# Optimization experiments

Measured on AMD Instinct MI355X. Metric: run time of the kernel, lower is better.

## Reference

```python
import jax, jax.numpy as jnp
import numpy as np

NUM_HEADS = 16
GROUP_SIZE = 4


def setup_inputs() -> dict:
    key = jax.random.key(0)
    k1, k2, k3 = jax.random.split(key, 3)
    B, N, C = 4, 8192, 1024
    x = jax.random.normal(k1, (B, N, C), dtype=jnp.float32)
    w_qkv = jax.random.normal(k2, (C, 3 * C), dtype=jnp.float32) * (C ** -0.5)
    w_proj = jax.random.normal(k3, (C, C), dtype=jnp.float32) * (C ** -0.5)
    b_proj = jnp.zeros((C,), dtype=jnp.float32)
    return {"x": x, "w_qkv": w_qkv, "w_proj": w_proj, "b_proj": b_proj, "causal": 0}


def reference(x, w_qkv, w_proj, b_proj, causal):
    # NOTE: the original non-flash path ignores `causal` (no mask applied).
    B, N, C = x.shape
    H, Dh, g = NUM_HEADS, C // NUM_HEADS, GROUP_SIZE
    G = N // g
    scale = Dh ** -0.5
    qkv = (x @ w_qkv).reshape(B, N, 3, H, Dh)
    q, k, v = qkv[:, :, 0], qkv[:, :, 1], qkv[:, :, 2]  # [B, N, H, Dh]
    # split sequence into G contiguous groups of size g
    q = q.reshape(B, G, g, H, Dh) * scale
    k = k.reshape(B, G, g, H, Dh)
    v = v.reshape(B, G, g, H, Dh)
    attn = jnp.einsum('bgnhd,bgmhd->bghnm', q, k)  # [B, G, H, g, g]
    attn = jax.nn.softmax(attn, axis=-1)
    o = jnp.einsum('bghnm,bgmhd->bgnhd', attn, v)  # [B, G, g, H, Dh]
    o = o.reshape(B, N, C)
    return o @ w_proj + b_proj
```

## Files before the change

kernel.cpp:

```cpp
#include <hip/hip_runtime.h>
#include <hip/hip_bf16.h>
#include <hip/hip_fp16.h>


typedef float    f32x4 __attribute__((ext_vector_type(4)));
typedef _Float16 f16x8 __attribute__((ext_vector_type(8)));
typedef _Float16 f16x4 __attribute__((ext_vector_type(4)));

__device__ __forceinline__ void gload16(const _Float16* g, _Float16* l) {
  __builtin_amdgcn_global_load_lds((const __attribute__((address_space(1))) void*)g,
                                   (__attribute__((address_space(3))) void*)l,
                                   16, 0, 0);
}

__global__ void wsplit_kernel(const float* __restrict__ W,
                              _Float16* __restrict__ BTh,
                              _Float16* __restrict__ BTl, int N) {
  __shared__ float tile[64][65];
  int n0 = blockIdx.x * 64;
  int k0 = blockIdx.y * 64;
  int t  = threadIdx.x;
  int tr = t >> 4, tc = t & 15;
#pragma unroll
  for (int it = 0; it < 4; ++it) {
    int k = k0 + tr + it * 16;
    f32x4 v = *reinterpret_cast<const f32x4*>(W + (size_t)k * N + n0 + (tc << 2));
#pragma unroll
    for (int c = 0; c < 4; ++c) tile[tr + it * 16][(tc << 2) + c] = v[c];
  }
  __syncthreads();
#pragma unroll
  for (int it = 0; it < 4; ++it) {
    int n = n0 + tr + it * 16;
    f16x4 hi, lo;
#pragma unroll
    for (int c = 0; c < 4; ++c) {
      float f = tile[(tc << 2) + c][tr + it * 16];
      _Float16 h = (_Float16)f;
      hi[c] = h;
      lo[c] = (_Float16)(f - (float)h);
    }
    size_t off = (size_t)n * 1024 + k0 + (tc << 2);
    *reinterpret_cast<f16x4*>(BTh + off) = hi;
    *reinterpret_cast<f16x4*>(BTl + off) = lo;
  }
}

__launch_bounds__(256)
__global__ void gemm_split_kernel(const float* __restrict__ A,
                                  const _Float16* __restrict__ Bh,
                                  const _Float16* __restrict__ Bl,
                                  float* __restrict__ C,
                                  const float* __restrict__ bias,
                                  int M, int N, int lda, int ldc) {
  __shared__ _Float16 lAh[128 * 32];
  __shared__ _Float16 lAl[128 * 32];
  __shared__ _Float16 lBh[128 * 32];
  __shared__ _Float16 lBl[128 * 32];

  int nwg = gridDim.x, bid = blockIdx.x;
  int q8  = nwg >> 3;
  int swz = (bid & 7) * q8 + (bid >> 3);
  int Mt  = M >> 7;
  int tm  = swz % Mt, tn = swz / Mt;
  int brow = tm << 7, bcol = tn << 7;

  int t  = threadIdx.x;
  int wv = t >> 6, lane = t & 63;
  int wrow = (wv >> 1) << 6;
  int wcol = (wv & 1) << 6;
  int lr = lane & 15, kb = lane >> 4;

  const float* paf = A + (size_t)(brow + (t >> 3)) * lda + ((t & 7) << 2);
  _Float16* wAh = lAh + (t >> 3) * 32 + ((t & 7) << 2);
  _Float16* wAl = lAl + (t >> 3) * 32 + ((t & 7) << 2);

  const _Float16* pbh0 = Bh + (size_t)(bcol + (t >> 2)) * 1024 + ((t & 3) << 3);
  const _Float16* pbh1 = pbh0 + (size_t)64 * 1024;
  const _Float16* pbl0 = Bl + (size_t)(bcol + (t >> 2)) * 1024 + ((t & 3) << 3);
  const _Float16* pbl1 = pbl0 + (size_t)64 * 1024;
  _Float16* lBh0 = lBh + wv * 512;
  _Float16* lBh1 = lBh + 2048 + wv * 512;
  _Float16* lBl0 = lBl + wv * 512;
  _Float16* lBl1 = lBl + 2048 + wv * 512;

  const _Float16* arh = lAh + (wrow + lr) * 32 + kb * 8;
  const _Float16* arl = lAl + (wrow + lr) * 32 + kb * 8;
  const _Float16* brh = lBh + (wcol + lr) * 32 + kb * 8;
  const _Float16* brl = lBl + (wcol + lr) * 32 + kb * 8;

  f32x4 acc[4][4] = {};

  for (int kt = 0; kt < 1024; kt += 32) {
#pragma unroll
    for (int p = 0; p < 4; ++p) {
      f32x4 v = *reinterpret_cast<const f32x4*>(paf + (size_t)(p * 32) * lda + kt);
      f16x4 h, l;
#pragma unroll
      for (int c = 0; c < 4; ++c) {
        _Float16 hh = (_Float16)v[c];
        h[c] = hh;
        l[c] = (_Float16)(v[c] - (float)hh);
      }
      *reinterpret_cast<f16x4*>(wAh + p * 1024) = h;
      *reinterpret_cast<f16x4*>(wAl + p * 1024) = l;
    }
    gload16(pbh0 + kt, lBh0);
    gload16(pbh1 + kt, lBh1);
    gload16(pbl0 + kt, lBl0);
    gload16(pbl1 + kt, lBl1);
    __syncthreads();

    f16x8 ah[4], al[4], bh[4], bl[4];
#pragma unroll
    for (int i = 0; i < 4; ++i) {
      ah[i] = *reinterpret_cast<const f16x8*>(arh + i * 512);
      al[i] = *reinterpret_cast<const f16x8*>(arl + i * 512);
      bh[i] = *reinterpret_cast<const f16x8*>(brh + i * 512);
      bl[i] = *reinterpret_cast<const f16x8*>(brl + i * 512);
    }
#pragma unroll
    for (int mi = 0; mi < 4; ++mi)
#pragma unroll
      for (int ni = 0; ni < 4; ++ni) {
        acc[mi][ni] = __builtin_amdgcn_mfma_f32_16x16x32_f16(ah[mi], bh[ni], acc[mi][ni], 0, 0, 0);
        acc[mi][ni] = __builtin_amdgcn_mfma_f32_16x16x32_f16(al[mi], bh[ni], acc[mi][ni], 0, 0, 0);
        acc[mi][ni] = __builtin_amdgcn_mfma_f32_16x16x32_f16(ah[mi], bl[ni], acc[mi][ni], 0, 0, 0);
      }
    __syncthreads();
  }

  int crow0 = brow + wrow + (kb << 2);
  int ccol0 = bcol + wcol + lr;
#pragma unroll
  for (int ni = 0; ni < 4; ++ni) {
    int col = ccol0 + (ni << 4);
    float bv = bias ? bias[col] : 0.0f;
#pragma unroll
    for (int mi = 0; mi < 4; ++mi) {
#pragma unroll
      for (int r = 0; r < 4; ++r) {
        int row = crow0 + (mi << 4) + r;
        C[(size_t)row * ldc + col] = acc[mi][ni][r] + bv;
      }
    }
  }
}

__global__ void attn_kernel(float* __restrict__ qkv) {
  int u    = (blockIdx.x << 2) + (threadIdx.x >> 6);
  int lane = threadIdx.x & 63;
  int j  = lane >> 4;
  int tq = lane & 15;
  int h   = u & 15;
  int grp = u >> 4;
  size_t row = (size_t)grp * 4 + j;
  size_t idx = row * 3072 + h * 64 + (tq << 2);

  f32x4 qv = *reinterpret_cast<const f32x4*>(qkv + idx);
  f32x4 kv = *reinterpret_cast<const f32x4*>(qkv + idx + 1024);
  f32x4 vv = *reinterpret_cast<const f32x4*>(qkv + idx + 2048);
  qv *= 0.125f;

  float s[4];
#pragma unroll
  for (int e = 0; e < 4; ++e) {
    f32x4 ke;
    if (e == 0) ke = kv;
    else {
#pragma unroll
      for (int c = 0; c < 4; ++c) ke[c] = __shfl_xor(kv[c], e << 4);
    }
    float p = qv[0]*ke[0] + qv[1]*ke[1] + qv[2]*ke[2] + qv[3]*ke[3];
    p += __shfl_xor(p, 1);
    p += __shfl_xor(p, 2);
    p += __shfl_xor(p, 4);
    p += __shfl_xor(p, 8);
    s[e] = p;
  }
  float mx = fmaxf(fmaxf(s[0], s[1]), fmaxf(s[2], s[3]));
  float e0 = expf(s[0] - mx), e1 = expf(s[1] - mx), e2 = expf(s[2] - mx), e3 = expf(s[3] - mx);
  float inv = 1.0f / (e0 + e1 + e2 + e3);
  float P[4] = {e0 * inv, e1 * inv, e2 * inv, e3 * inv};

  f32x4 o = {0.0f, 0.0f, 0.0f, 0.0f};
#pragma unroll
  for (int e = 0; e < 4; ++e) {
    f32x4 ve;
    if (e == 0) ve = vv;
    else {
#pragma unroll
      for (int c = 0; c < 4; ++c) ve[c] = __shfl_xor(vv[c], e << 4);
    }
    o += P[e] * ve;
  }

  *reinterpret_cast<f32x4*>(qkv + idx) = o;
}

extern "C" void kernel_launch(void* const* d_in, const int* in_sizes, int n_in,
                              void* d_out, int out_size, void* d_ws, size_t ws_size,
                              hipStream_t stream) {
  const float* x      = (const float*)d_in[0];
  const float* w_qkv  = (const float*)d_in[1];
  const float* w_proj = (const float*)d_in[2];
  const float* b_proj = (const float*)d_in[3];
  float* out = (float*)d_out;
  char* ws = (char*)d_ws;

  int Ms;
  if      (ws_size >= 117440512ull) Ms = 8192;
  else if (ws_size >=  41943040ull) Ms = 2048;
  else                              Ms = 512;
  const int SL = 32768 / Ms;

  size_t qkvBytes = (size_t)Ms * 3072 * 4;
  float*    QKVs = (float*)ws;
  _Float16* Bqh  = (_Float16*)(ws + qkvBytes);
  _Float16* Bql  = (_Float16*)(ws + qkvBytes + 6291456ull);
  _Float16* Bph  = (_Float16*)(ws + qkvBytes + 12582912ull);
  _Float16* Bpl  = (_Float16*)(ws + qkvBytes + 14680064ull);

  wsplit_kernel<<<dim3(48, 16), 256, 0, stream>>>(w_qkv, Bqh, Bql, 3072);
  wsplit_kernel<<<dim3(16, 16), 256, 0, stream>>>(w_proj, Bph, Bpl, 1024);

  for (int s = 0; s < SL; ++s) {
    const float* xs = x + (size_t)s * Ms * 1024;
    gemm_split_kernel<<<(Ms >> 7) * 24, 256, 0, stream>>>(
        xs, Bqh, Bql, QKVs, nullptr, Ms, 3072, 1024, 3072);
    attn_kernel<<<Ms, 256, 0, stream>>>(QKVs);
    gemm_split_kernel<<<(Ms >> 7) * 8, 256, 0, stream>>>(
        QKVs, Bph, Bpl, out + (size_t)s * Ms * 1024, b_proj, Ms, 1024, 3072, 1024);
  }
}
```

Measured before the change: 1.195 ms.

## Presplit activations to fp16 hi/lo and add pipelined 256x256 QKV GEMM

Adds a pre-pass that splits x into interleaved fp16 hi/lo planes, so the QKV GEMM no longer converts fp32 inside its main loop. The QKV GEMM is replaced by a 512-thread, 256x256-tile kernel with 4-slot LDS multi-buffering, swizzled LDS layout, explicit vmcnt waits and setprio around MFMA. The 3-term split product runs as a 48-step K loop over the concatenated hi/lo planes. Attention now writes its output directly as fp16 hi/lo for the projection GEMM, and the projection GEMM does three sequential passes over the planes. The workspace chunk sizes are also changed, and the extra split pass costs additional memory traffic.

Measured after the change: 1.623 ms. +35.8%, slower.

```diff
diff --git a/kernel.cpp b/kernel.cpp
--- a/kernel.cpp
+++ b/kernel.cpp
@@ -13,14 +13,29 @@
                                    16, 0, 0);
 }
 
+#define FULL_BAR() do { asm volatile("" ::: "memory"); \
+  __builtin_amdgcn_s_barrier(); asm volatile("" ::: "memory"); } while (0)
+
+__global__ void presplit_kernel(const float* __restrict__ x, _Float16* __restrict__ XA) {
+  int gid = blockIdx.x * 256 + threadIdx.x;
+  int row = gid >> 8, c4 = gid & 255;
+  f32x4 v = *reinterpret_cast<const f32x4*>(x + ((size_t)gid << 2));
+  f16x4 hi, lo;
+#pragma unroll
+  for (int c = 0; c < 4; ++c) {
+    _Float16 h = (_Float16)v[c];
+    hi[c] = h; lo[c] = (_Float16)(v[c] - (float)h);
+  }
+  size_t o = (size_t)row * 2048 + (c4 << 2);
+  *reinterpret_cast<f16x4*>(XA + o)        = hi;
+  *reinterpret_cast<f16x4*>(XA + o + 1024) = lo;
+}
+
 __global__ void wsplit_kernel(const float* __restrict__ W,
-                              _Float16* __restrict__ BTh,
-                              _Float16* __restrict__ BTl, int N) {
+                              _Float16* __restrict__ BT, int N) {
   __shared__ float tile[64][65];
-  int n0 = blockIdx.x * 64;
-  int k0 = blockIdx.y * 64;
-  int t  = threadIdx.x;
-  int tr = t >> 4, tc = t & 15;
+  int n0 = blockIdx.x * 64, k0 = blockIdx.y * 64;
+  int t = threadIdx.x, tr = t >> 4, tc = t & 15;
 #pragma unroll
   for (int it = 0; it < 4; ++it) {
     int k = k0 + tr + it * 16;
@@ -37,97 +52,193 @@
     for (int c = 0; c < 4; ++c) {
       float f = tile[(tc << 2) + c][tr + it * 16];
       _Float16 h = (_Float16)f;
-      hi[c] = h;
-      lo[c] = (_Float16)(f - (float)h);
-    }
-    size_t off = (size_t)n * 1024 + k0 + (tc << 2);
-    *reinterpret_cast<f16x4*>(BTh + off) = hi;
-    *reinterpret_cast<f16x4*>(BTl + off) = lo;
-  }
+      hi[c] = h; lo[c] = (_Float16)(f - (float)h);
+    }
+    size_t off = (size_t)n * 2048 + k0 + (tc << 2);
+    *reinterpret_cast<f16x4*>(BT + off)        = hi;
+    *reinterpret_cast<f16x4*>(BT + off + 1024) = lo;
+  }
+}
+
+__launch_bounds__(512, 1)
+__global__ void gemm8_kernel(const _Float16* __restrict__ A,
+                             const _Float16* __restrict__ B,
+                             float* __restrict__ C, int M) {
+  __shared__ _Float16 lds[65536];
+
+  int nwg = gridDim.x, bid = blockIdx.x;
+  int q = nwg >> 3, r = nwg & 7, xcd = bid & 7, loc = bid >> 3;
+  int swz = (xcd < r ? xcd * (q + 1) : r * (q + 1) + (xcd - r) * q) + loc;
+  int Mt = M >> 8;
+  int tm = swz % Mt, tn = swz / Mt;
+  int brow = tm << 8, bcol = tn << 8;
+
+  int t = threadIdx.x;
+  int wid = t >> 6, lane = t & 63;
+  int wm = wid >> 2, wn = wid & 3;
+  int lr = lane & 15, kb = lane >> 4;
+
+  auto stage = [&](int isB, int KT, int kh) {
+    int plane = isB ? (((KT >> 4) == 2) ? 1024 : 0) : (((KT >> 4) == 1) ? 1024 : 0);
+    int kbase = plane + (KT & 15) * 64 + kh * 32;
+    const _Float16* src = isB ? B : A;
+    int rowBase = isB ? bcol : brow;
+    _Float16* slot = lds + (isB ? 32768 : 0) + (((2 * KT + kh) & 3) << 13);
+#pragma unroll
+    for (int qq = 0; qq < 2; ++qq) {
+      int p = (qq << 9) | t;
+      int row = p >> 2;
+      int cc = (p & 3) ^ (row & 3);
+      gload16(src + (size_t)(rowBase + row) * 2048 + kbase + (cc << 3),
+              slot + (((qq << 9) | (wid << 6)) << 3));
+    }
+  };
+
+  int aSwz = (kb ^ (lr & 3)) << 3;
+  int aRow = (wm * 128 + lr) * 32 + aSwz;
+  int bRow = (wn * 64 + lr) * 32 + aSwz;
+
+  f32x4 acc[8][4] = {};
+
+  stage(1, 0, 0); stage(0, 0, 0); stage(1, 0, 1); stage(0, 0, 1);
+  stage(1, 1, 0); stage(0, 1, 0);
+  asm volatile("s_waitcnt vmcnt(4)" ::: "memory");
+  FULL_BAR();
+
+  for (int KT = 0; KT < 48; ++KT) {
+    const _Float16* sA0 = lds + (((2 * KT) & 3) << 13);
+    const _Float16* sA1 = lds + (((2 * KT + 1) & 3) << 13);
+    const _Float16* sB0 = lds + 32768 + (((2 * KT) & 3) << 13);
+    const _Float16* sB1 = lds + 32768 + (((2 * KT + 1) & 3) << 13);
+    f16x8 aq[4], bq[4];
+
+#pragma unroll
+    for (int i = 0; i < 4; ++i) aq[i] = *reinterpret_cast<const f16x8*>(sA0 + aRow + i * 512);
+#pragma unroll
+    for (int i = 0; i < 4; ++i) bq[i] = *reinterpret_cast<const f16x8*>(sB0 + bRow + i * 512);
+    if (KT + 1 < 48) stage(1, KT + 1, 1);
+    FULL_BAR();
+    __builtin_amdgcn_s_setprio(1);
+#pragma unroll
+    for (int mi = 0; mi < 4; ++mi)
+#pragma unroll
+      for (int ni = 0; ni < 4; ++ni)
+        acc[mi][ni] = __builtin_amdgcn_mfma_f32_16x16x32_f16(aq[mi], bq[ni], acc[mi][ni], 0, 0, 0);
+    __builtin_amdgcn_s_setprio(0);
+    FULL_BAR();
+
+#pragma unroll
+    for (int i = 0; i < 4; ++i) aq[i] = *reinterpret_cast<const f16x8*>(sA0 + aRow + (i + 4) * 512);
+    if (KT + 1 < 48) stage(0, KT + 1, 1);
+    FULL_BAR();
+    __builtin_amdgcn_s_setprio(1);
+#pragma unroll
+    for (int mi = 0; mi < 4; ++mi)
+#pragma unroll
+      for (int ni = 0; ni < 4; ++ni)
+        acc[mi + 4][ni] = __builtin_amdgcn_mfma_f32_16x16x32_f16(aq[mi], bq[ni], acc[mi + 4][ni], 0, 0, 0);
+    __builtin_amdgcn_s_setprio(0);
+    FULL_BAR();
+
+#pragma unroll
+    for (int i = 0; i < 4; ++i) aq[i] = *reinterpret_cast<const f16x8*>(sA1 + aRow + i * 512);
+#pragma unroll
+    for (int i = 0; i < 4; ++i) bq[i] = *reinterpret_cast<const f16x8*>(sB1 + bRow + i * 512);
+    if (KT + 2 < 48) stage(1, KT + 2, 0);
+    FULL_BAR();
+    __builtin_amdgcn_s_setprio(1);
+#pragma unroll
+    for (int mi = 0; mi < 4; ++mi)
+#pragma unroll
+      for (int ni = 0; ni < 4; ++ni)
+        acc[mi][ni] = __builtin_amdgcn_mfma_f32_16x16x32_f16(aq[mi], bq[ni], acc[mi][ni], 0, 0, 0);
+    __builtin_amdgcn_s_setprio(0);
+    FULL_BAR();
+
+#pragma unroll
+    for (int i = 0; i < 4; ++i) aq[i] = *reinterpret_cast<const f16x8*>(sA1 + aRow + (i + 4) * 512);
+    if (KT + 2 < 48) stage(0, KT + 2, 0);
+    FULL_BAR();
+    __builtin_amdgcn_s_setprio(1);
+#pragma unroll
+    for (int mi = 0; mi < 4; ++mi)
+#pragma unroll
+      for (int ni = 0; ni < 4; ++ni)
+        acc[mi + 4][ni] = __builtin_amdgcn_mfma_f32_16x16x32_f16(aq[mi], bq[ni], acc[mi + 4][ni], 0, 0, 0);
+    __builtin_amdgcn_s_setprio(0);
+    if (KT < 46) asm volatile("s_waitcnt vmcnt(4)" ::: "memory");
+    else         asm volatile("s_waitcnt vmcnt(0)" ::: "memory");
+    FULL_BAR();
+  }
+
+  int crow0 = brow + wm * 128 + (kb << 2);
+  int ccol0 = bcol + wn * 64 + lr;
+#pragma unroll
+  for (int mi = 0; mi < 8; ++mi)
+#pragma unroll
+    for (int ni = 0; ni < 4; ++ni)
+#pragma unroll
+      for (int rr = 0; rr < 4; ++rr)
+        C[(size_t)(crow0 + mi * 16 + rr) * 3072 + ccol0 + ni * 16] = acc[mi][ni][rr];
 }
 
 __launch_bounds__(256)
-__global__ void gemm_split_kernel(const float* __restrict__ A,
-                                  const _Float16* __restrict__ Bh,
-                                  const _Float16* __restrict__ Bl,
-                                  float* __restrict__ C,
-                                  const float* __restrict__ bias,
-                                  int M, int N, int lda, int ldc) {
-  __shared__ _Float16 lAh[128 * 32];
-  __shared__ _Float16 lAl[128 * 32];
-  __shared__ _Float16 lBh[128 * 32];
-  __shared__ _Float16 lBl[128 * 32];
+__global__ void gemm3_kernel(const _Float16* __restrict__ A,
+                             const _Float16* __restrict__ B,
+                             void* __restrict__ Cptr,
+                             const float* __restrict__ bias, int c16,
+                             int M, int N, int ldc) {
+  __shared__ _Float16 lA[128 * 32];
+  __shared__ _Float16 lB[128 * 32];
 
   int nwg = gridDim.x, bid = blockIdx.x;
-  int q8  = nwg >> 3;
+  int q8 = nwg >> 3;
   int swz = (bid & 7) * q8 + (bid >> 3);
-  int Mt  = M >> 7;
-  int tm  = swz % Mt, tn = swz / Mt;
+  int Mt = M >> 7;
+  int tm = swz % Mt, tn = swz / Mt;
   int brow = tm << 7, bcol = tn << 7;
 
-  int t  = threadIdx.x;
+  int t = threadIdx.x;
   int wv = t >> 6, lane = t & 63;
-  int wrow = (wv >> 1) << 6;
-  int wcol = (wv & 1) << 6;
+  int wrow = (wv >> 1) << 6, wcol = (wv & 1) << 6;
   int lr = lane & 15, kb = lane >> 4;
 
-  const float* paf = A + (size_t)(brow + (t >> 3)) * lda + ((t & 7) << 2);
-  _Float16* wAh = lAh + (t >> 3) * 32 + ((t & 7) << 2);
-  _Float16* wAl = lAl + (t >> 3) * 32 + ((t & 7) << 2);
-
-  const _Float16* pbh0 = Bh + (size_t)(bcol + (t >> 2)) * 1024 + ((t & 3) << 3);
-  const _Float16* pbh1 = pbh0 + (size_t)64 * 1024;
-  const _Float16* pbl0 = Bl + (size_t)(bcol + (t >> 2)) * 1024 + ((t & 3) << 3);
-  const _Float16* pbl1 = pbl0 + (size_t)64 * 1024;
-  _Float16* lBh0 = lBh + wv * 512;
-  _Float16* lBh1 = lBh + 2048 + wv * 512;
-  _Float16* lBl0 = lBl + wv * 512;
-  _Float16* lBl1 = lBl + 2048 + wv * 512;
-
-  const _Float16* arh = lAh + (wrow + lr) * 32 + kb * 8;
-  const _Float16* arl = lAl + (wrow + lr) * 32 + kb * 8;
-  const _Float16* brh = lBh + (wcol + lr) * 32 + kb * 8;
-  const _Float16* brl = lBl + (wcol + lr) * 32 + kb * 8;
+  const _Float16* pa0 = A + (size_t)(brow + (t >> 2)) * 2048 + ((t & 3) << 3);
+  const _Float16* pa1 = pa0 + (size_t)64 * 2048;
+  const _Float16* pb0 = B + (size_t)(bcol + (t >> 2)) * 2048 + ((t & 3) << 3);
+  const _Float16* pb1 = pb0 + (size_t)64 * 2048;
+  _Float16* lA0 = lA + wv * 512;
+  _Float16* lA1 = lA + 2048 + wv * 512;
+  _Float16* lB0 = lB + wv * 512;
+  _Float16* lB1 = lB + 2048 + wv * 512;
+
+  const _Float16* ar = lA + (wrow + lr) * 32 + kb * 8;
+  const _Float16* br = lB + (wcol + lr) * 32 + kb * 8;
 
   f32x4 acc[4][4] = {};
 
-  for (int kt = 0; kt < 1024; kt += 32) {
-#pragma unroll
-    for (int p = 0; p < 4; ++p) {
-      f32x4 v = *reinterpret_cast<const f32x4*>(paf + (size_t)(p * 32) * lda + kt);
-      f16x4 h, l;
-#pragma unroll
-      for (int c = 0; c < 4; ++c) {
-        _Float16 hh = (_Float16)v[c];
-        h[c] = hh;
-        l[c] = (_Float16)(v[c] - (float)hh);
+  for (int pass = 0; pass < 3; ++pass) {
+    int aOff = (pass == 1) ? 1024 : 0;
+    int bOff = (pass == 2) ? 1024 : 0;
+    for (int kt = 0; kt < 1024; kt += 32) {
+      gload16(pa0 + aOff + kt, lA0);
+      gload16(pa1 + aOff + kt, lA1);
+      gload16(pb0 + bOff + kt, lB0);
+      gload16(pb1 + bOff + kt, lB1);
+      __syncthreads();
+      f16x8 af[4], bf[4];
+#pragma unroll
+      for (int i = 0; i < 4; ++i) {
+        af[i] = *reinterpret_cast<const f16x8*>(ar + i * 512);
+        bf[i] = *reinterpret_cast<const f16x8*>(br + i * 512);
       }
-      *reinterpret_cast<f16x4*>(wAh + p * 1024) = h;
-      *reinterpret_cast<f16x4*>(wAl + p * 1024) = l;
-    }
-    gload16(pbh0 + kt, lBh0);
-    gload16(pbh1 + kt, lBh1);
-    gload16(pbl0 + kt, lBl0);
-    gload16(pbl1 + kt, lBl1);
-    __syncthreads();
-
-    f16x8 ah[4], al[4], bh[4], bl[4];
-#pragma unroll
-    for (int i = 0; i < 4; ++i) {
-      ah[i] = *reinterpret_cast<const f16x8*>(arh + i * 512);
-      al[i] = *reinterpret_cast<const f16x8*>(arl + i * 512);
-      bh[i] = *reinterpret_cast<const f16x8*>(brh + i * 512);
-      bl[i] = *reinterpret_cast<const f16x8*>(brl + i * 512);
-    }
-#pragma unroll
-    for (int mi = 0; mi < 4; ++mi)
-#pragma unroll
-      for (int ni = 0; ni < 4; ++ni) {
-        acc[mi][ni] = __builtin_amdgcn_mfma_f32_16x16x32_f16(ah[mi], bh[ni], acc[mi][ni], 0, 0, 0);
-        acc[mi][ni] = __builtin_amdgcn_mfma_f32_16x16x32_f16(al[mi], bh[ni], acc[mi][ni], 0, 0, 0);
-        acc[mi][ni] = __builtin_amdgcn_mfma_f32_16x16x32_f16(ah[mi], bl[ni], acc[mi][ni], 0, 0, 0);
-      }
-    __syncthreads();
+#pragma unroll
+      for (int mi = 0; mi < 4; ++mi)
+#pragma unroll
+        for (int ni = 0; ni < 4; ++ni)
+          acc[mi][ni] = __builtin_amdgcn_mfma_f32_16x16x32_f16(af[mi], bf[ni], acc[mi][ni], 0, 0, 0);
+      __syncthreads();
+    }
   }
 
   int crow0 = brow + wrow + (kb << 2);
@@ -135,25 +246,26 @@
 #pragma unroll
   for (int ni = 0; ni < 4; ++ni) {
     int col = ccol0 + (ni << 4);
-    float bv = bias ? bias[col] : 0.0f;
+    float bv = (!c16 && bias) ? bias[col] : 0.0f;
 #pragma unroll
     for (int mi = 0; mi < 4; ++mi) {
 #pragma unroll
-      for (int r = 0; r < 4; ++r) {
-        int row = crow0 + (mi << 4) + r;
-        C[(size_t)row * ldc + col] = acc[mi][ni][r] + bv;
+      for (int rr = 0; rr < 4; ++rr) {
+        int row = crow0 + (mi << 4) + rr;
+        if (c16)
+          ((_Float16*)Cptr)[(size_t)row * ldc + col] = (_Float16)acc[mi][ni][rr];
+        else
+          ((float*)Cptr)[(size_t)row * ldc + col] = acc[mi][ni][rr] + bv;
       }
     }
   }
 }
 
-__global__ void attn_kernel(float* __restrict__ qkv) {
-  int u    = (blockIdx.x << 2) + (threadIdx.x >> 6);
+__global__ void attn_kernel(const float* __restrict__ qkv, _Float16* __restrict__ XA) {
+  int u = (blockIdx.x << 2) + (threadIdx.x >> 6);
   int lane = threadIdx.x & 63;
-  int j  = lane >> 4;
-  int tq = lane & 15;
-  int h   = u & 15;
-  int grp = u >> 4;
+  int j = lane >> 4, tq = lane & 15;
+  int h = u & 15, grp = u >> 4;
   size_t row = (size_t)grp * 4 + j;
   size_t idx = row * 3072 + h * 64 + (tq << 2);
 
@@ -179,9 +291,9 @@
     s[e] = p;
   }
   float mx = fmaxf(fmaxf(s[0], s[1]), fmaxf(s[2], s[3]));
-  float e0 = expf(s[0] - mx), e1 = expf(s[1] - mx), e2 = expf(s[2] - mx), e3 = expf(s[3] - mx);
+  float e0 = expf(s[0]-mx), e1 = expf(s[1]-mx), e2 = expf(s[2]-mx), e3 = expf(s[3]-mx);
   float inv = 1.0f / (e0 + e1 + e2 + e3);
-  float P[4] = {e0 * inv, e1 * inv, e2 * inv, e3 * inv};
+  float P[4] = {e0*inv, e1*inv, e2*inv, e3*inv};
 
   f32x4 o = {0.0f, 0.0f, 0.0f, 0.0f};
 #pragma unroll
@@ -195,7 +307,15 @@
     o += P[e] * ve;
   }
 
-  *reinterpret_cast<f32x4*>(qkv + idx) = o;
+  f16x4 hi, lo;
+#pragma unroll
+  for (int c = 0; c < 4; ++c) {
+    _Float16 hh = (_Float16)o[c];
+    hi[c] = hh; lo[c] = (_Float16)(o[c] - (float)hh);
+  }
+  size_t oo = row * 2048 + h * 64 + (tq << 2);
+  *reinterpret_cast<f16x4*>(XA + oo)        = hi;
+  *reinterpret_cast<f16x4*>(XA + oo + 1024) = lo;
 }
 
 extern "C" void kernel_launch(void* const* d_in, const int* in_sizes, int n_in,
@@ -209,27 +329,27 @@
   char* ws = (char*)d_ws;
 
   int Ms;
-  if      (ws_size >= 117440512ull) Ms = 8192;
-  else if (ws_size >=  41943040ull) Ms = 2048;
-  else                              Ms = 512;
+  if      (ws_size >= 83886080ull) Ms = 4096;
+  else if (ws_size >= 33554432ull) Ms = 1024;
+  else                             Ms = 256;
   const int SL = 32768 / Ms;
 
-  size_t qkvBytes = (size_t)Ms * 3072 * 4;
-  float*    QKVs = (float*)ws;
-  _Float16* Bqh  = (_Float16*)(ws + qkvBytes);
-  _Float16* Bql  = (_Float16*)(ws + qkvBytes + 6291456ull);
-  _Float16* Bph  = (_Float16*)(ws + qkvBytes + 12582912ull);
-  _Float16* Bpl  = (_Float16*)(ws + qkvBytes + 14680064ull);
-
-  wsplit_kernel<<<dim3(48, 16), 256, 0, stream>>>(w_qkv, Bqh, Bql, 3072);
-  wsplit_kernel<<<dim3(16, 16), 256, 0, stream>>>(w_proj, Bph, Bpl, 1024);
+  size_t sXA  = (size_t)Ms * 2048 * 2;
+  size_t sQKV = (size_t)Ms * 3072 * 4;
+  _Float16* XA  = (_Float16*)ws;
+  float*    QKV = (float*)(ws + sXA);
+  _Float16* Bq  = (_Float16*)(ws + sXA + sQKV);
+  _Float16* Bp  = (_Float16*)(ws + sXA + sQKV + 12582912ull);
+
+  wsplit_kernel<<<dim3(48, 16), 256, 0, stream>>>(w_qkv, Bq, 3072);
+  wsplit_kernel<<<dim3(16, 16), 256, 0, stream>>>(w_proj, Bp, 1024);
 
   for (int s = 0; s < SL; ++s) {
     const float* xs = x + (size_t)s * Ms * 1024;
-    gemm_split_kernel<<<(Ms >> 7) * 24, 256, 0, stream>>>(
-        xs, Bqh, Bql, QKVs, nullptr, Ms, 3072, 1024, 3072);
-    attn_kernel<<<Ms, 256, 0, stream>>>(QKVs);
-    gemm_split_kernel<<<(Ms >> 7) * 8, 256, 0, stream>>>(
-        QKVs, Bph, Bpl, out + (size_t)s * Ms * 1024, b_proj, Ms, 1024, 3072, 1024);
-  }
-}
+    presplit_kernel<<<Ms, 256, 0, stream>>>(xs, XA);
+    gemm8_kernel<<<(Ms >> 8) * 12, 512, 0, stream>>>(XA, Bq, QKV, Ms);
+    attn_kernel<<<Ms, 256, 0, stream>>>(QKV, XA);
+    gemm3_kernel<<<(Ms >> 7) * 8, 256, 0, stream>>>(
+        XA, Bp, out + (size_t)s * Ms * 1024, b_proj, 0, Ms, 1024, 1024);
+  }
+}
```
